# Performance work log

Hardware: AMD Instinct MI355X
Metric: run time of the kernel (lower is better)

## Reference

```python
import jax, jax.numpy as jnp
import numpy as np


def _max_agg_conv(x, w, b, src, dst, num_nodes):
    # Linear transform then gather along source nodes and scatter-max to targets.
    h = x @ w.T + b                      # [N, out]
    msgs = h[src]                        # [E, out] edge messages (x_j)
    agg = jax.ops.segment_max(msgs, dst, num_segments=num_nodes)  # [N, out]
    # torch_scatter / PyG fill isolated nodes with 0, jax fills with -inf
    return jnp.where(jnp.isneginf(agg), jnp.zeros((), agg.dtype), agg)


def setup_inputs() -> dict:
    key = jax.random.key(0)
    k_x, k_e, k_w1, k_b1, k_w2, k_b2 = jax.random.split(key, 6)
    N, E = 100000, 1600000
    IN, HID, OUT = 128, 32, 32
    x = jax.random.normal(k_x, (N, IN), dtype=jnp.float32)
    edge_index = jax.random.randint(k_e, (2, E), 0, N, dtype=jnp.int64)
    s1 = 1.0 / np.sqrt(IN)
    s2 = 1.0 / np.sqrt(HID)
    w1 = jax.random.uniform(k_w1, (HID, IN), jnp.float32, -s1, s1)
    b1 = jax.random.uniform(k_b1, (HID,), jnp.float32, -s1, s1)
    w2 = jax.random.uniform(k_w2, (OUT, HID), jnp.float32, -s2, s2)
    b2 = jax.random.uniform(k_b2, (OUT,), jnp.float32, -s2, s2)
    return {"x": x, "edge_index": edge_index, "w1": w1, "b1": b1, "w2": w2, "b2": b2}


def reference(x, edge_index, w1, b1, w2, b2):
    num_nodes = x.shape[0]
    src, dst = edge_index[0], edge_index[1]
    h = _max_agg_conv(x, w1, b1, src, dst, num_nodes)   # conv1
    h = jax.nn.relu(h)
    out = _max_agg_conv(h, w2, b2, src, dst, num_nodes)  # conv2
    return out
```

## Files before the change

### kernel.cpp

```cpp
#include <hip/hip_runtime.h>
#include <math.h>


#define NPB 512
#define BSHIFT 9
#define CAP 32
#define CCH 8192

__global__ __launch_bounds__(256) void fill_s32_kernel(int* __restrict__ p, int v, int n) {
    int i = blockIdx.x * 256 + threadIdx.x;
    if (i < n) p[i] = v;
}

__global__ __launch_bounds__(256) void hist_buckets_kernel(
    const int* __restrict__ dst, int* __restrict__ bcnt, int B, int E)
{
    __shared__ int lc[256];
    const int tid = threadIdx.x;
    lc[tid] = 0;
    __syncthreads();
    for (int e = blockIdx.x * 256 + tid; e < E; e += gridDim.x * 256)
        atomicAdd(&lc[dst[e] >> BSHIFT], 1);
    __syncthreads();
    if (tid < B && lc[tid]) atomicAdd(&bcnt[tid], lc[tid]);
}

__global__ __launch_bounds__(256) void bucket_scan_kernel(
    int* __restrict__ bcur, int* __restrict__ bbase, int* __restrict__ of_cnt,
    int B, int E)
{
    __shared__ int sh[256];
    const int tid = threadIdx.x;
    int v = (tid < B) ? bcur[tid] : 0;
    sh[tid] = v;
    __syncthreads();
    #pragma unroll
    for (int d = 1; d < 256; d <<= 1) {
        int t = (tid >= d) ? sh[tid - d] : 0;
        __syncthreads();
        sh[tid] += t;
        __syncthreads();
    }
    if (tid < B) { int b = sh[tid] - v; bbase[tid] = b; bcur[tid] = b; }
    if (tid == 0) { bbase[B] = E; *of_cnt = 0; }
}

__global__ __launch_bounds__(256) void partition_kernel(
    const int* __restrict__ src, const int* __restrict__ dst,
    int* __restrict__ bcur, uint2* __restrict__ pairs, int E)
{
    __shared__ uint2 stage[CCH];
    __shared__ int lcnt[256], loffs[256], lcur[256], gb[256], sh[256];
    const int tid = threadIdx.x;
    const int e0 = blockIdx.x * CCH;
    const int ecnt = min(CCH, E - e0);
    lcnt[tid] = 0;
    __syncthreads();
    for (int i = tid; i < ecnt; i += 256)
        atomicAdd(&lcnt[dst[e0 + i] >> BSHIFT], 1);
    __syncthreads();
    int v = lcnt[tid];
    sh[tid] = v;
    __syncthreads();
    #pragma unroll
    for (int d = 1; d < 256; d <<= 1) {
        int t = (tid >= d) ? sh[tid - d] : 0;
        __syncthreads();
        sh[tid] += t;
        __syncthreads();
    }
    loffs[tid] = sh[tid] - v;
    lcur[tid] = sh[tid] - v;
    gb[tid] = v ? atomicAdd(&bcur[tid], v) : 0;
    __syncthreads();
    for (int i = tid; i < ecnt; i += 256) {
        int d = dst[e0 + i];
        int s = atomicAdd(&lcur[d >> BSHIFT], 1);
        stage[s] = make_uint2((unsigned)src[e0 + i], (unsigned)d);
    }
    __syncthreads();
    for (int i = tid; i < ecnt; i += 256) {
        uint2 p = stage[i];
        int b = (int)(p.y >> BSHIFT);
        pairs[gb[b] + (i - loffs[b])] = p;
    }
}

__global__ __launch_bounds__(256) void build_ell_kernel(
    const uint2* __restrict__ pairs, const int* __restrict__ bbase,
    int* __restrict__ ell, int* __restrict__ cnt,
    uint2* __restrict__ of_list, int* __restrict__ of_cnt, int N, int of_cap)
{
    __shared__ int lcnt[NPB];
    __shared__ int lell[NPB * CAP];
    const int tid = threadIdx.x, b = blockIdx.x;
    for (int i = tid; i < NPB; i += 256) lcnt[i] = 0;
    __syncthreads();
    const int p0 = bbase[b], p1 = bbase[b + 1];
    for (int i = p0 + tid; i < p1; i += 256) {
        uint2 p = pairs[i];
        int ln = (int)p.y - b * NPB;
        int s = atomicAdd(&lcnt[ln], 1);
        if (s < CAP) lell[ln * CAP + s] = (int)p.x;
        else { int oi = atomicAdd(of_cnt, 1); if (oi < of_cap) of_list[oi] = p; }
    }
    __syncthreads();
    const size_t eb = (size_t)b * NPB * CAP;
    for (int i = tid; i < NPB * CAP; i += 256) ell[eb + i] = lell[i];
    const int n0 = b * NPB;
    for (int i = tid; i < NPB; i += 256)
        if (n0 + i < N) cnt[n0 + i] = lcnt[i];
}

__global__ __launch_bounds__(256) void linear1_kernel(
    const float* __restrict__ x, const float* __restrict__ w1,
    const float* __restrict__ b1, float* __restrict__ h1, int N)
{
    __shared__ float wsh[32][132];
    __shared__ float xs[32][128];
    const int tid = threadIdx.x;
    for (int i = tid; i < 32 * 128; i += 256) wsh[i >> 7][i & 127] = w1[i];
    const int node0 = blockIdx.x * 32;
    const float4* x4 = reinterpret_cast<const float4*>(x + (size_t)node0 * 128);
    for (int q = tid; q < 32 * 32; q += 256) {
        int row = q >> 5;
        if (node0 + row < N) {
            float4 v = x4[q];
            *reinterpret_cast<float4*>(&xs[row][(q & 31) * 4]) = v;
        }
    }
    __syncthreads();
    const int g = tid >> 5, j = tid & 31;
    const int nb = g * 4;
    const float bj = b1[j];
    float acc[4] = {bj, bj, bj, bj};
    const float4* wrow = reinterpret_cast<const float4*>(&wsh[j][0]);
    #pragma unroll 4
    for (int k4 = 0; k4 < 32; ++k4) {
        float4 w = wrow[k4];
        #pragma unroll
        for (int a = 0; a < 4; ++a) {
            float4 xv = *reinterpret_cast<const float4*>(&xs[nb + a][k4 * 4]);
            acc[a] += xv.x * w.x + xv.y * w.y + xv.z * w.z + xv.w * w.w;
        }
    }
    #pragma unroll
    for (int a = 0; a < 4; ++a) {
        int n = node0 + nb + a;
        if (n < N) h1[(size_t)n * 32 + j] = acc[a];
    }
}

__global__ __launch_bounds__(256) void linear2_kernel(
    const float* __restrict__ agg1, const float* __restrict__ w2,
    const float* __restrict__ b2, float* __restrict__ h2, int N)
{
    __shared__ float wsh[32][36];
    __shared__ float rs[64][32];
    const int tid = threadIdx.x;
    for (int i = tid; i < 32 * 32; i += 256) wsh[i >> 5][i & 31] = w2[i];
    const int node0 = blockIdx.x * 64;
    const float4* a4 = reinterpret_cast<const float4*>(agg1 + (size_t)node0 * 32);
    for (int q = tid; q < 64 * 8; q += 256) {
        int row = q >> 3;
        if (node0 + row < N) {
            float4 v = a4[q];
            *reinterpret_cast<float4*>(&rs[row][(q & 7) * 4]) = v;
        }
    }
    __syncthreads();
    const int g = tid >> 5, j = tid & 31;
    const int nb = g * 8;
    const float bj = b2[j];
    float acc[8];
    #pragma unroll
    for (int a = 0; a < 8; ++a) acc[a] = bj;
    const float4* wrow = reinterpret_cast<const float4*>(&wsh[j][0]);
    #pragma unroll
    for (int k4 = 0; k4 < 8; ++k4) {
        float4 w = wrow[k4];
        #pragma unroll
        for (int a = 0; a < 8; ++a) {
            float4 xv = *reinterpret_cast<const float4*>(&rs[nb + a][k4 * 4]);
            acc[a] += xv.x * w.x + xv.y * w.y + xv.z * w.z + xv.w * w.w;
        }
    }
    #pragma unroll
    for (int a = 0; a < 8; ++a) {
        int n = node0 + nb + a;
        if (n < N) h2[(size_t)n * 32 + j] = acc[a];
    }
}

__global__ __launch_bounds__(256) void agg_ell_kernel(
    const float* __restrict__ h, const int* __restrict__ cnt,
    const int* __restrict__ ell, float* __restrict__ out,
    int N, float seed, int fixup)
{
    int t = blockIdx.x * 256 + threadIdx.x;
    int n = t >> 3;
    if (n >= N) return;
    int c = (t & 7) << 2;
    int total = cnt[n];
    int deg = min(total, CAP);
    const int* row = ell + (size_t)n * CAP;
    float4 acc = {seed, seed, seed, seed};
    int k = 0;
    for (; k + 1 < deg; k += 2) {
        int s0 = row[k], s1 = row[k + 1];
        float4 v0 = *reinterpret_cast<const float4*>(h + (size_t)s0 * 32 + c);
        float4 v1 = *reinterpret_cast<const float4*>(h + (size_t)s1 * 32 + c);
        acc.x = fmaxf(acc.x, fmaxf(v0.x, v1.x));
        acc.y = fmaxf(acc.y, fmaxf(v0.y, v1.y));
        acc.z = fmaxf(acc.z, fmaxf(v0.z, v1.z));
        acc.w = fmaxf(acc.w, fmaxf(v0.w, v1.w));
    }
    if (k < deg) {
        int s0 = row[k];
        float4 v0 = *reinterpret_cast<const float4*>(h + (size_t)s0 * 32 + c);
        acc.x = fmaxf(acc.x, v0.x);
        acc.y = fmaxf(acc.y, v0.y);
        acc.z = fmaxf(acc.z, v0.z);
        acc.w = fmaxf(acc.w, v0.w);
    }
    if (fixup && total == 0) acc = make_float4(0.f, 0.f, 0.f, 0.f);
    *reinterpret_cast<float4*>(out + (size_t)n * 32 + c) = acc;
}

__device__ __forceinline__ void atomicMaxF(float* a, float v) {
    int* ai = (int*)a;
    int old = *ai;
    while (v > __int_as_float(old)) {
        int assumed = old;
        old = atomicCAS(ai, assumed, __float_as_int(v));
        if (old == assumed) break;
    }
}

__global__ __launch_bounds__(256) void overflow_fixup_kernel(
    const float* __restrict__ h, const uint2* __restrict__ of_list,
    const int* __restrict__ of_cnt, float* __restrict__ out, int of_cap)
{
    int m = min(*of_cnt, of_cap);
    for (int t = blockIdx.x * 256 + threadIdx.x; t < m * 8; t += gridDim.x * 256) {
        int e = t >> 3, c = (t & 7) << 2;
        uint2 p = of_list[e];
        const float* hv = h + (size_t)p.x * 32 + c;
        float* a = out + (size_t)p.y * 32 + c;
        atomicMaxF(a + 0, hv[0]);
        atomicMaxF(a + 1, hv[1]);
        atomicMaxF(a + 2, hv[2]);
        atomicMaxF(a + 3, hv[3]);
    }
}

extern "C" void kernel_launch(void* const* d_in, const int* in_sizes, int n_in,
                              void* d_out, int out_size, void* d_ws, size_t ws_size,
                              hipStream_t stream)
{
    const float* x  = (const float*)d_in[0];
    const int*   ei = (const int*)d_in[1];
    const float* w1 = (const float*)d_in[2];
    const float* b1 = (const float*)d_in[3];
    const float* w2 = (const float*)d_in[4];
    const float* b2 = (const float*)d_in[5];
    float* out = (float*)d_out;

    const int N = in_sizes[0] / 128;
    const int E = in_sizes[1] / 2;
    const int C = (int)((size_t)N * 32);
    const int B = (N + NPB - 1) / NPB;
    const int* src = ei;
    const int* dst = ei + E;

    auto align256 = [](size_t v) { return (v + 255) & ~(size_t)255; };
    size_t off = 0;
    size_t rsize = (size_t)C * 4 > (size_t)E * 8 ? (size_t)C * 4 : (size_t)E * 8;
    char* base = (char*)d_ws;
    uint2* pairs = (uint2*)(base + off);
    float* bufA  = (float*)(base + off);       off = align256(off + rsize);
    float* bufB  = (float*)(base + off);       off = align256(off + (size_t)C * 4);
    int*   ell   = (int*)(base + off);         off = align256(off + (size_t)B * NPB * CAP * 4);
    int*   cnt   = (int*)(base + off);         off = align256(off + (size_t)N * 4);
    int*   bbase = (int*)(base + off);         off = align256(off + (size_t)(B + 1) * 4);
    int*   bcur  = (int*)(base + off);         off = align256(off + (size_t)B * 4);
    int*   of_cnt = (int*)(base + off);        off = align256(off + 256);
    uint2* of_list = (uint2*)(base + off);
    size_t rem = (ws_size > off) ? (ws_size - off) / 8 : 0;
    int of_cap = (int)((rem < (size_t)E) ? rem : (size_t)E);

    fill_s32_kernel<<<(B + 255) / 256, 256, 0, stream>>>(bcur, 0, B);
    hist_buckets_kernel<<<256, 256, 0, stream>>>(dst, bcur, B, E);
    bucket_scan_kernel<<<1, 256, 0, stream>>>(bcur, bbase, of_cnt, B, E);
    partition_kernel<<<(E + CCH - 1) / CCH, 256, 0, stream>>>(src, dst, bcur, pairs, E);
    build_ell_kernel<<<B, 256, 0, stream>>>(pairs, bbase, ell, cnt, of_list, of_cnt, N, of_cap);

    const int aggGrid = (int)(((size_t)N * 8 + 255) / 256);

    linear1_kernel<<<(N + 31) / 32, 256, 0, stream>>>(x, w1, b1, bufA, N);
    agg_ell_kernel<<<aggGrid, 256, 0, stream>>>(bufA, cnt, ell, bufB, N, 0.0f, 0);
    overflow_fixup_kernel<<<32, 256, 0, stream>>>(bufA, of_list, of_cnt, bufB, of_cap);

    linear2_kernel<<<(N + 63) / 64, 256, 0, stream>>>(bufB, w2, b2, bufA, N);
    agg_ell_kernel<<<aggGrid, 256, 0, stream>>>(bufA, cnt, ell, out, N, -INFINITY, 1);
    overflow_fixup_kernel<<<32, 256, 0, stream>>>(bufA, of_list, of_cnt, out, of_cap);
}
```

Before: 288.6 us.

## Use split-bf16 MFMA for first linear, pad bucket counters, shrink partition chunks

Replaces the scalar FP32 first linear layer with an MFMA kernel that splits x and w1 into high and low bf16 parts and sums three bf16 products, approximating FP32 accuracy on matrix cores. Bucket cursor counters are padded 16 ints apart so global atomics from many blocks do not land on the same cache lines. The partition chunk size drops from 8192 to 2048 edges, giving more blocks and less shared memory per block. The split-bf16 path drops the low-by-low product, so results differ slightly from plain FP32.

```diff
diff --git a/kernel.cpp b/kernel.cpp
--- a/kernel.cpp
+++ b/kernel.cpp
@@ -5,7 +5,11 @@
 #define NPB 512
 #define BSHIFT 9
 #define CAP 32
-#define CCH 8192
+#define CCH 2048
+#define BPAD 16
+
+typedef __attribute__((ext_vector_type(8))) short bf16x8;
+typedef __attribute__((ext_vector_type(4))) float f32x4;
 
 __global__ __launch_bounds__(256) void fill_s32_kernel(int* __restrict__ p, int v, int n) {
     int i = blockIdx.x * 256 + threadIdx.x;
@@ -22,7 +26,7 @@
     for (int e = blockIdx.x * 256 + tid; e < E; e += gridDim.x * 256)
         atomicAdd(&lc[dst[e] >> BSHIFT], 1);
     __syncthreads();
-    if (tid < B && lc[tid]) atomicAdd(&bcnt[tid], lc[tid]);
+    if (tid < B && lc[tid]) atomicAdd(&bcnt[tid * BPAD], lc[tid]);
 }
 
 __global__ __launch_bounds__(256) void bucket_scan_kernel(
@@ -31,7 +35,7 @@
 {
     __shared__ int sh[256];
     const int tid = threadIdx.x;
-    int v = (tid < B) ? bcur[tid] : 0;
+    int v = (tid < B) ? bcur[tid * BPAD] : 0;
     sh[tid] = v;
     __syncthreads();
     #pragma unroll
@@ -41,7 +45,7 @@
         sh[tid] += t;
         __syncthreads();
     }
-    if (tid < B) { int b = sh[tid] - v; bbase[tid] = b; bcur[tid] = b; }
+    if (tid < B) { int b = sh[tid] - v; bbase[tid] = b; bcur[tid * BPAD] = b; }
     if (tid == 0) { bbase[B] = E; *of_cnt = 0; }
 }
 
@@ -71,7 +75,7 @@
     }
     loffs[tid] = sh[tid] - v;
     lcur[tid] = sh[tid] - v;
-    gb[tid] = v ? atomicAdd(&bcur[tid], v) : 0;
+    gb[tid] = v ? atomicAdd(&bcur[tid * BPAD], v) : 0;
     __syncthreads();
     for (int i = tid; i < ecnt; i += 256) {
         int d = dst[e0 + i];
@@ -112,42 +116,87 @@
         if (n0 + i < N) cnt[n0 + i] = lcnt[i];
 }
 
-__global__ __launch_bounds__(256) void linear1_kernel(
+__device__ __forceinline__ void split_bf16(float f, unsigned short& hi, unsigned short& lo) {
+    unsigned u = __float_as_uint(f);
+    hi = (unsigned short)(u >> 16);
+    float fh = __uint_as_float(u & 0xffff0000u);
+    float r = f - fh;
+    lo = (unsigned short)(__float_as_uint(r) >> 16);
+}
+
+#define L1S 136
+__global__ __launch_bounds__(256) void linear1_mfma_kernel(
     const float* __restrict__ x, const float* __restrict__ w1,
     const float* __restrict__ b1, float* __restrict__ h1, int N)
 {
-    __shared__ float wsh[32][132];
-    __shared__ float xs[32][128];
-    const int tid = threadIdx.x;
-    for (int i = tid; i < 32 * 128; i += 256) wsh[i >> 7][i & 127] = w1[i];
-    const int node0 = blockIdx.x * 32;
-    const float4* x4 = reinterpret_cast<const float4*>(x + (size_t)node0 * 128);
+    __shared__ unsigned short xh[64 * L1S];
+    __shared__ unsigned short xl[64 * L1S];
+    __shared__ unsigned short wh[32 * L1S];
+    __shared__ unsigned short wl[32 * L1S];
+    const int tid = threadIdx.x;
+    const int node0 = blockIdx.x * 64;
     for (int q = tid; q < 32 * 32; q += 256) {
-        int row = q >> 5;
+        int row = q >> 5, qc = (q & 31) * 4;
+        float4 v = *reinterpret_cast<const float4*>(w1 + row * 128 + qc);
+        unsigned short h0, l0, h1s, l1s, h2, l2, h3, l3;
+        split_bf16(v.x, h0, l0); split_bf16(v.y, h1s, l1s);
+        split_bf16(v.z, h2, l2); split_bf16(v.w, h3, l3);
+        short4 hv = {(short)h0, (short)h1s, (short)h2, (short)h3};
+        short4 lv = {(short)l0, (short)l1s, (short)l2, (short)l3};
+        *reinterpret_cast<short4*>(&wh[row * L1S + qc]) = hv;
+        *reinterpret_cast<short4*>(&wl[row * L1S + qc]) = lv;
+    }
+    for (int q = tid; q < 64 * 32; q += 256) {
+        int row = q >> 5, qc = (q & 31) * 4;
         if (node0 + row < N) {
-            float4 v = x4[q];
-            *reinterpret_cast<float4*>(&xs[row][(q & 31) * 4]) = v;
-        }
-    }
-    __syncthreads();
-    const int g = tid >> 5, j = tid & 31;
-    const int nb = g * 4;
-    const float bj = b1[j];
-    float acc[4] = {bj, bj, bj, bj};
-    const float4* wrow = reinterpret_cast<const float4*>(&wsh[j][0]);
-    #pragma unroll 4
-    for (int k4 = 0; k4 < 32; ++k4) {
-        float4 w = wrow[k4];
+            float4 v = *reinterpret_cast<const float4*>(x + (size_t)(node0 + row) * 128 + qc);
+            unsigned short h0, l0, h1s, l1s, h2, l2, h3, l3;
+            split_bf16(v.x, h0, l0); split_bf16(v.y, h1s, l1s);
+            split_bf16(v.z, h2, l2); split_bf16(v.w, h3, l3);
+            short4 hv = {(short)h0, (short)h1s, (short)h2, (short)h3};
+            short4 lv = {(short)l0, (short)l1s, (short)l2, (short)l3};
+            *reinterpret_cast<short4*>(&xh[row * L1S + qc]) = hv;
+            *reinterpret_cast<short4*>(&xl[row * L1S + qc]) = lv;
+        }
+    }
+    __syncthreads();
+    const int wid = tid >> 6, lane = tid & 63;
+    const int arow = wid * 16 + (lane & 15);
+    const int koff = (lane >> 4) * 8;
+    bf16x8 ah[4], al[4], bh[2][4], bl[2][4];
+    #pragma unroll
+    for (int kt = 0; kt < 4; ++kt) {
+        ah[kt] = *reinterpret_cast<const bf16x8*>(&xh[arow * L1S + kt * 32 + koff]);
+        al[kt] = *reinterpret_cast<const bf16x8*>(&xl[arow * L1S + kt * 32 + koff]);
+    }
+    #pragma unroll
+    for (int nt = 0; nt < 2; ++nt) {
+        int ch = nt * 16 + (lane & 15);
         #pragma unroll
-        for (int a = 0; a < 4; ++a) {
-            float4 xv = *reinterpret_cast<const float4*>(&xs[nb + a][k4 * 4]);
-            acc[a] += xv.x * w.x + xv.y * w.y + xv.z * w.z + xv.w * w.w;
-        }
-    }
-    #pragma unroll
-    for (int a = 0; a < 4; ++a) {
-        int n = node0 + nb + a;
-        if (n < N) h1[(size_t)n * 32 + j] = acc[a];
+        for (int kt = 0; kt < 4; ++kt) {
+            bh[nt][kt] = *reinterpret_cast<const bf16x8*>(&wh[ch * L1S + kt * 32 + koff]);
+            bl[nt][kt] = *reinterpret_cast<const bf16x8*>(&wl[ch * L1S + kt * 32 + koff]);
+        }
+    }
+    f32x4 acc[2] = {{0.f, 0.f, 0.f, 0.f}, {0.f, 0.f, 0.f, 0.f}};
+    #pragma unroll
+    for (int nt = 0; nt < 2; ++nt)
+        #pragma unroll
+        for (int kt = 0; kt < 4; ++kt) {
+            acc[nt] = __builtin_amdgcn_mfma_f32_16x16x32_bf16(ah[kt], bh[nt][kt], acc[nt], 0, 0, 0);
+            acc[nt] = __builtin_amdgcn_mfma_f32_16x16x32_bf16(ah[kt], bl[nt][kt], acc[nt], 0, 0, 0);
+            acc[nt] = __builtin_amdgcn_mfma_f32_16x16x32_bf16(al[kt], bh[nt][kt], acc[nt], 0, 0, 0);
+        }
+    const int col = lane & 15, r0 = (lane >> 4) * 4;
+    #pragma unroll
+    for (int nt = 0; nt < 2; ++nt) {
+        int ch = nt * 16 + col;
+        float bias = b1[ch];
+        #pragma unroll
+        for (int r = 0; r < 4; ++r) {
+            int n = node0 + wid * 16 + r0 + r;
+            if (n < N) h1[(size_t)n * 32 + ch] = acc[nt][r] + bias;
+        }
     }
 }
 
@@ -283,13 +332,13 @@
     int*   ell   = (int*)(base + off);         off = align256(off + (size_t)B * NPB * CAP * 4);
     int*   cnt   = (int*)(base + off);         off = align256(off + (size_t)N * 4);
     int*   bbase = (int*)(base + off);         off = align256(off + (size_t)(B + 1) * 4);
-    int*   bcur  = (int*)(base + off);         off = align256(off + (size_t)B * 4);
+    int*   bcur  = (int*)(base + off);         off = align256(off + (size_t)B * BPAD * 4);
     int*   of_cnt = (int*)(base + off);        off = align256(off + 256);
     uint2* of_list = (uint2*)(base + off);
     size_t rem = (ws_size > off) ? (ws_size - off) / 8 : 0;
     int of_cap = (int)((rem < (size_t)E) ? rem : (size_t)E);
 
-    fill_s32_kernel<<<(B + 255) / 256, 256, 0, stream>>>(bcur, 0, B);
+    fill_s32_kernel<<<(B * BPAD + 255) / 256, 256, 0, stream>>>(bcur, 0, B * BPAD);
     hist_buckets_kernel<<<256, 256, 0, stream>>>(dst, bcur, B, E);
     bucket_scan_kernel<<<1, 256, 0, stream>>>(bcur, bbase, of_cnt, B, E);
     partition_kernel<<<(E + CCH - 1) / CCH, 256, 0, stream>>>(src, dst, bcur, pairs, E);
@@ -297,7 +346,7 @@
 
     const int aggGrid = (int)(((size_t)N * 8 + 255) / 256);
 
-    linear1_kernel<<<(N + 31) / 32, 256, 0, stream>>>(x, w1, b1, bufA, N);
+    linear1_mfma_kernel<<<(N + 63) / 64, 256, 0, stream>>>(x, w1, b1, bufA, N);
     agg_ell_kernel<<<aggGrid, 256, 0, stream>>>(bufA, cnt, ell, bufB, N, 0.0f, 0);
     overflow_fixup_kernel<<<32, 256, 0, stream>>>(bufA, of_list, of_cnt, bufB, of_cap);
 
```

New measurement: 271.6 us. -5.9%, faster.
